# Kernel tuning notes

Hardware: AMD Instinct MI355X
Metric: run time of the kernel (lower is better)

The kernel has to match this reference:

```python
import jax, jax.numpy as jnp
import numpy as np

B, H, S, DK, DV = 2, 8, 2048, 64, 64


def _alibi_bias(num_heads, q_len, k_len, dtype=jnp.float32):
    # standard ALiBi slopes: 2^(-8h/H) for h = 1..H
    slopes = 2.0 ** (-8.0 * jnp.arange(1, num_heads + 1, dtype=dtype) / num_heads)
    # relative distance bias: -(i - j), zero on/above diagonal matters only pre-mask
    dist = jnp.arange(k_len, dtype=dtype)[None, :] - jnp.arange(q_len, dtype=dtype)[:, None]
    return (slopes[:, None, None] * dist[None, :, :])[None]  # (1, H, S, S)


def setup_inputs() -> dict:
    key = jax.random.key(0)
    kq, kk, kv = jax.random.split(key, 3)
    query = jax.random.normal(kq, (B, H, S, DK), dtype=jnp.float32)
    key_t = jax.random.normal(kk, (B, H, S, DK), dtype=jnp.float32)
    value = jax.random.normal(kv, (B, H, S, DV), dtype=jnp.float32)
    # causal mask: positions with 1 are masked (j > i)
    mask = jnp.triu(jnp.ones((S, S), dtype=jnp.int32), k=1)[None, None]  # (1,1,S,S)
    alibi_bias = _alibi_bias(H, S, S)  # (1,H,S,S)
    return {"query": query, "key": key_t, "value": value, "mask": mask, "alibi_bias": alibi_bias}


def reference(query, key, value, mask, alibi_bias):
    d_k = query.shape[-1]
    scale = 1.0 / jnp.sqrt(jnp.asarray(d_k, dtype=jnp.float32))
    # scores: (B, H, S, S)
    scores = jnp.einsum("bhqd,bhkd->bhqk", query, key) * scale
    scores = scores + alibi_bias
    scores = jnp.where(mask == 1, -jnp.inf, scores)
    attention_weights = jax.nn.softmax(scores, axis=-1)
    output = jnp.einsum("bhqk,bhkd->bhqd", attention_weights, value)
    return output, attention_weights
```

## Files before the change

### kernel.cpp

```cpp
#include <hip/hip_runtime.h>
#include <math.h>

#define BB 2
#define HH 8
#define SS 2048
#define DD 64
#define NBH (BB*HH)

typedef float f32x4 __attribute__((ext_vector_type(4)));
typedef short bf16x8 __attribute__((ext_vector_type(8)));
typedef short bf16x4 __attribute__((ext_vector_type(4)));

static __device__ __forceinline__ short f2bf(float x) {
    unsigned u = __float_as_uint(x);
    u = (u + 0x7fffu + ((u >> 16) & 1u)) >> 16;
    return (short)u;
}

__global__ __launch_bounds__(256) void prep_qk(const float* __restrict__ Q,
                                               const float* __restrict__ K,
                                               short* __restrict__ Qb,
                                               short* __restrict__ Kb)
{
    const int n4 = NBH * SS * DD / 4;
    for (int idx = blockIdx.x * 256 + threadIdx.x; idx < n4; idx += gridDim.x * 256) {
        float4 q = ((const float4*)Q)[idx];
        float4 k = ((const float4*)K)[idx];
        bf16x4 qo, ko;
        qo[0] = f2bf(0.125f * q.x); qo[1] = f2bf(0.125f * q.y);
        qo[2] = f2bf(0.125f * q.z); qo[3] = f2bf(0.125f * q.w);
        ko[0] = f2bf(k.x); ko[1] = f2bf(k.y); ko[2] = f2bf(k.z); ko[3] = f2bf(k.w);
        ((bf16x4*)Qb)[idx] = qo;
        ((bf16x4*)Kb)[idx] = ko;
    }
}

__global__ __launch_bounds__(256) void prep_vt(const float* __restrict__ V,
                                               short* __restrict__ Vt)
{
    __shared__ short t[64][72];
    const int jt = blockIdx.x, bh = blockIdx.y;
    const int tid = threadIdx.x;
    const int r  = tid >> 2;
    const int c4 = (tid & 3) * 16;
    const float* vb = V + ((size_t)bh * SS + (size_t)jt * 64) * DD;
    #pragma unroll
    for (int cc = 0; cc < 4; ++cc) {
        float4 v = *(const float4*)(vb + r * DD + c4 + cc * 4);
        t[c4 + cc*4 + 0][r] = f2bf(v.x);
        t[c4 + cc*4 + 1][r] = f2bf(v.y);
        t[c4 + cc*4 + 2][r] = f2bf(v.z);
        t[c4 + cc*4 + 3][r] = f2bf(v.w);
    }
    __syncthreads();
    short* ob = Vt + ((size_t)bh * DD + r) * SS + (size_t)jt * 64 + c4;
    *(bf16x8*)ob       = *(bf16x8*)&t[r][c4];
    *(bf16x8*)(ob + 8) = *(bf16x8*)&t[r][c4 + 8];
}

__global__ __launch_bounds__(512, 4) void attn_main(
    const short* __restrict__ Qb, const short* __restrict__ Kb,
    const short* __restrict__ Vt,
    float* __restrict__ out, float* __restrict__ wts)
{
    const int flat = blockIdx.x;
    const int wg   = (flat & 7) * 128 + (flat >> 3);
    const int bh   = wg >> 6;
    const int t_   = wg & 63;
    const int qt   = (t_ < 32) ? t_ : 95 - t_;
    const int q0   = qt * 32;
    const int h    = bh & 7;

    const int tid  = threadIdx.x;
    const int wv   = tid >> 6;
    const int lane = tid & 63;
    const int g    = lane >> 4;
    const int c16  = lane & 15;

    __shared__ float smo[8][16][65];
    __shared__ float lred[8][2][16];

    const short* Qp = Qb + ((size_t)bh * SS + q0) * DD;
    const short* Kp = Kb + (size_t)bh * SS * DD;
    const short* Vp = Vt + (size_t)bh * DD * SS;
    float* wbase = wts + ((size_t)bh * SS + q0) * (size_t)SS;
    float* obase = out + ((size_t)bh * SS + q0) * DD;

    const float slope  = exp2f(-(float)(h + 1));
    const int   nsteps = qt + 1;
    const int   cover  = q0 + 32;

    {
        const int n4 = (SS - cover) >> 2;
        const f32x4 z = {0.f, 0.f, 0.f, 0.f};
        for (int r = 0; r < 32; ++r) {
            float* wr = wbase + (size_t)r * SS + cover;
            for (int c = tid; c < n4; c += 512) ((f32x4*)wr)[c] = z;
        }
    }

    bf16x8 qf[2][2];
    #pragma unroll
    for (int qh = 0; qh < 2; ++qh)
        #pragma unroll
        for (int c = 0; c < 2; ++c)
            qf[qh][c] = *(const bf16x8*)(Qp + (size_t)(qh*16 + c16) * DD + c*32 + g*8);

    int kk8[8]; float offc[8];
    #pragma unroll
    for (int t = 0; t < 2; ++t)
        #pragma unroll
        for (int r = 0; r < 4; ++r) {
            kk8[t*4+r]  = 16*t + 4*g + r;
            offc[t*4+r] = slope * (float)(16*t + 4*g + r);
        }

    float l[2] = {0.f, 0.f};
    for (int s = wv; s < nsteps; s += 8) {
        const int j0 = s * 32;
        bf16x8 kf[2][2];
        #pragma unroll
        for (int t = 0; t < 2; ++t)
            #pragma unroll
            for (int c = 0; c < 2; ++c)
                kf[t][c] = *(const bf16x8*)(Kp + (size_t)(j0 + 16*t + c16) * DD + c*32 + g*8);

        f32x4 acc[2][2];
        #pragma unroll
        for (int qh = 0; qh < 2; ++qh)
            #pragma unroll
            for (int t = 0; t < 2; ++t)
                acc[qh][t] = (f32x4){0.f, 0.f, 0.f, 0.f};
        #pragma unroll
        for (int qh = 0; qh < 2; ++qh)
            #pragma unroll
            for (int t = 0; t < 2; ++t)
                #pragma unroll
                for (int c = 0; c < 2; ++c)
                    acc[qh][t] = __builtin_amdgcn_mfma_f32_16x16x32_bf16(kf[t][c], qf[qh][c], acc[qh][t], 0, 0, 0);

        const bool diag = (s == qt);
        #pragma unroll
        for (int qh = 0; qh < 2; ++qh) {
            const int   irow = q0 + qh*16 + c16;
            const float sb   = slope * (float)(j0 - irow);
            const int   lim  = irow - j0;
            float ls = 0.f;
            #pragma unroll
            for (int u = 0; u < 8; ++u) {
                float e = __expf(acc[qh][u>>2][u&3] + sb + offc[u]);
                if (diag) e = (kk8[u] <= lim) ? e : 0.f;
                ls += e;
            }
            l[qh] += ls;
        }
    }
    #pragma unroll
    for (int qh = 0; qh < 2; ++qh) {
        l[qh] += __shfl_xor(l[qh], 16, 64);
        l[qh] += __shfl_xor(l[qh], 32, 64);
    }

    if (lane < 16) {
        #pragma unroll
        for (int qh = 0; qh < 2; ++qh) lred[wv][qh][lane] = l[qh];
    }
    __syncthreads();
    float invl[2];
    #pragma unroll
    for (int qh = 0; qh < 2; ++qh) {
        float lf = 0.f;
        #pragma unroll
        for (int w2 = 0; w2 < 8; ++w2) lf += lred[w2][qh][c16];
        invl[qh] = 1.f / lf;
    }

    f32x4 oacc[2][4];
    #pragma unroll
    for (int qh = 0; qh < 2; ++qh)
        #pragma unroll
        for (int d0 = 0; d0 < 4; ++d0) oacc[qh][d0] = (f32x4){0.f, 0.f, 0.f, 0.f};

    for (int s = wv; s < nsteps; s += 8) {
        const int j0 = s * 32;
        bf16x8 kf[2][2];
        #pragma unroll
        for (int t = 0; t < 2; ++t)
            #pragma unroll
            for (int c = 0; c < 2; ++c)
                kf[t][c] = *(const bf16x8*)(Kp + (size_t)(j0 + 16*t + c16) * DD + c*32 + g*8);

        f32x4 acc[2][2];
        #pragma unroll
        for (int qh = 0; qh < 2; ++qh)
            #pragma unroll
            for (int t = 0; t < 2; ++t)
                acc[qh][t] = (f32x4){0.f, 0.f, 0.f, 0.f};
        #pragma unroll
        for (int qh = 0; qh < 2; ++qh)
            #pragma unroll
            for (int t = 0; t < 2; ++t)
                #pragma unroll
                for (int c = 0; c < 2; ++c)
                    acc[qh][t] = __builtin_amdgcn_mfma_f32_16x16x32_bf16(kf[t][c], qf[qh][c], acc[qh][t], 0, 0, 0);

        const bool diag = (s == qt);
        bf16x8 wf[2];
        #pragma unroll
        for (int qh = 0; qh < 2; ++qh) {
            const int   irow = q0 + qh*16 + c16;
            const float sb   = slope * (float)(j0 - irow);
            const int   lim  = irow - j0;
            float w8[8];
            #pragma unroll
            for (int u = 0; u < 8; ++u) {
                float e = __expf(acc[qh][u>>2][u&3] + sb + offc[u]);
                if (diag) e = (kk8[u] <= lim) ? e : 0.f;
                w8[u] = e * invl[qh];
            }
            float* wr0 = wbase + (size_t)(qh*16 + c16) * SS + j0 + 4*g;
            *(f32x4*)wr0        = (f32x4){w8[0], w8[1], w8[2], w8[3]};
            *(f32x4*)(wr0 + 16) = (f32x4){w8[4], w8[5], w8[6], w8[7]};
            #pragma unroll
            for (int u = 0; u < 8; ++u) wf[qh][u] = f2bf(w8[u]);
        }

        const short* vp = Vp + j0;
        #pragma unroll
        for (int d0 = 0; d0 < 4; ++d0) {
            const short* vr = vp + (size_t)(d0*16 + c16) * SS;
            bf16x4 a  = *(const bf16x4*)(vr + 4*g);
            bf16x4 b2 = *(const bf16x4*)(vr + 16 + 4*g);
            bf16x8 vf;
            vf[0]=a[0]; vf[1]=a[1]; vf[2]=a[2]; vf[3]=a[3];
            vf[4]=b2[0]; vf[5]=b2[1]; vf[6]=b2[2]; vf[7]=b2[3];
            #pragma unroll
            for (int qh = 0; qh < 2; ++qh)
                oacc[qh][d0] = __builtin_amdgcn_mfma_f32_16x16x32_bf16(vf, wf[qh], oacc[qh][d0], 0, 0, 0);
        }
    }

    __syncthreads();
    #pragma unroll
    for (int qh = 0; qh < 2; ++qh) {
        #pragma unroll
        for (int d0 = 0; d0 < 4; ++d0)
            *(f32x4*)&smo[wv][c16][d0*16 + 4*g] = oacc[qh][d0];
        __syncthreads();
        if (tid < 256) {
            int q = tid >> 4, dc = tid & 15;
            f32x4 r = {0.f, 0.f, 0.f, 0.f};
            #pragma unroll
            for (int w2 = 0; w2 < 8; ++w2) r += *(f32x4*)&smo[w2][q][dc * 4];
            *(f32x4*)(obase + (size_t)(qh*16 + q) * DD + dc * 4) = r;
        }
        __syncthreads();
    }
}

extern "C" void kernel_launch(void* const* d_in, const int* in_sizes, int n_in,
                              void* d_out, int out_size, void* d_ws, size_t ws_size,
                              hipStream_t stream) {
    const float* Q = (const float*)d_in[0];
    const float* K = (const float*)d_in[1];
    const float* V = (const float*)d_in[2];

    float* out = (float*)d_out;
    float* wts = out + (size_t)BB * HH * SS * DD;

    const size_t n = (size_t)NBH * SS * DD;
    short* Qb = (short*)d_ws;
    short* Kb = Qb + n;
    short* Vt = Kb + n;

    prep_qk<<<dim3(1024), dim3(256), 0, stream>>>(Q, K, Qb, Kb);
    prep_vt<<<dim3(SS / 64, NBH), dim3(256), 0, stream>>>(V, Vt);

    attn_main<<<dim3(1024), dim3(512), 0, stream>>>(Qb, Kb, Vt, out, wts);
}
```

Before: 120.7 us.

## Split query tiles into paired 16-row groups per workgroup

Each workgroup now processes two 16-row query groups (G and 127-G) sequentially instead of one 32-row tile, rebalancing causal work at finer granularity. Per-step computation handles a single 16-row Q fragment, reducing register pressure. In exchange, K and V fragments are reused across fewer rows, and the kernel adds an extra pass with its own synchronizations and partially masked diagonal blocks.

```diff
diff --git a/kernel.cpp b/kernel.cpp
--- a/kernel.cpp
+++ b/kernel.cpp
@@ -66,9 +66,7 @@
     const int flat = blockIdx.x;
     const int wg   = (flat & 7) * 128 + (flat >> 3);
     const int bh   = wg >> 6;
-    const int t_   = wg & 63;
-    const int qt   = (t_ < 32) ? t_ : 95 - t_;
-    const int q0   = qt * 32;
+    const int slot = wg & 63;
     const int h    = bh & 7;
 
     const int tid  = threadIdx.x;
@@ -78,33 +76,12 @@
     const int c16  = lane & 15;
 
     __shared__ float smo[8][16][65];
-    __shared__ float lred[8][2][16];
-
-    const short* Qp = Qb + ((size_t)bh * SS + q0) * DD;
+    __shared__ float lred[8][16];
+
     const short* Kp = Kb + (size_t)bh * SS * DD;
     const short* Vp = Vt + (size_t)bh * DD * SS;
-    float* wbase = wts + ((size_t)bh * SS + q0) * (size_t)SS;
-    float* obase = out + ((size_t)bh * SS + q0) * DD;
-
-    const float slope  = exp2f(-(float)(h + 1));
-    const int   nsteps = qt + 1;
-    const int   cover  = q0 + 32;
-
-    {
-        const int n4 = (SS - cover) >> 2;
-        const f32x4 z = {0.f, 0.f, 0.f, 0.f};
-        for (int r = 0; r < 32; ++r) {
-            float* wr = wbase + (size_t)r * SS + cover;
-            for (int c = tid; c < n4; c += 512) ((f32x4*)wr)[c] = z;
-        }
-    }
-
-    bf16x8 qf[2][2];
-    #pragma unroll
-    for (int qh = 0; qh < 2; ++qh)
-        #pragma unroll
-        for (int c = 0; c < 2; ++c)
-            qf[qh][c] = *(const bf16x8*)(Qp + (size_t)(qh*16 + c16) * DD + c*32 + g*8);
+
+    const float slope = exp2f(-(float)(h + 1));
 
     int kk8[8]; float offc[8];
     #pragma unroll
@@ -115,144 +92,137 @@
             offc[t*4+r] = slope * (float)(16*t + 4*g + r);
         }
 
-    float l[2] = {0.f, 0.f};
-    for (int s = wv; s < nsteps; s += 8) {
-        const int j0 = s * 32;
-        bf16x8 kf[2][2];
-        #pragma unroll
-        for (int t = 0; t < 2; ++t)
-            #pragma unroll
-            for (int c = 0; c < 2; ++c)
-                kf[t][c] = *(const bf16x8*)(Kp + (size_t)(j0 + 16*t + c16) * DD + c*32 + g*8);
-
-        f32x4 acc[2][2];
-        #pragma unroll
-        for (int qh = 0; qh < 2; ++qh)
-            #pragma unroll
-            for (int t = 0; t < 2; ++t)
-                acc[qh][t] = (f32x4){0.f, 0.f, 0.f, 0.f};
-        #pragma unroll
-        for (int qh = 0; qh < 2; ++qh)
-            #pragma unroll
-            for (int t = 0; t < 2; ++t)
-                #pragma unroll
-                for (int c = 0; c < 2; ++c)
-                    acc[qh][t] = __builtin_amdgcn_mfma_f32_16x16x32_bf16(kf[t][c], qf[qh][c], acc[qh][t], 0, 0, 0);
-
-        const bool diag = (s == qt);
-        #pragma unroll
-        for (int qh = 0; qh < 2; ++qh) {
-            const int   irow = q0 + qh*16 + c16;
-            const float sb   = slope * (float)(j0 - irow);
-            const int   lim  = irow - j0;
+    #pragma unroll 1
+    for (int it = 0; it < 2; ++it) {
+        const int G      = (it == 0) ? slot : 127 - slot;
+        const int q0     = G * 16;
+        const int nsteps = (G >> 1) + 1;
+        const int cover  = nsteps * 32;
+        const int irow   = q0 + c16;
+
+        const short* Qp = Qb + ((size_t)bh * SS + q0) * DD;
+        float* wbase = wts + ((size_t)bh * SS + q0) * (size_t)SS;
+        float* obase = out + ((size_t)bh * SS + q0) * DD;
+
+        {
+            const int n4 = (SS - cover) >> 2;
+            const f32x4 z = {0.f, 0.f, 0.f, 0.f};
+            for (int r = 0; r < 16; ++r) {
+                float* wr = wbase + (size_t)r * SS + cover;
+                for (int c = tid; c < n4; c += 512) ((f32x4*)wr)[c] = z;
+            }
+        }
+
+        bf16x8 qf[2];
+        #pragma unroll
+        for (int c = 0; c < 2; ++c)
+            qf[c] = *(const bf16x8*)(Qp + (size_t)c16 * DD + c*32 + g*8);
+
+        float l = 0.f;
+        for (int s = wv; s < nsteps; s += 8) {
+            const int j0 = s * 32;
+            bf16x8 kf[2][2];
+            #pragma unroll
+            for (int t = 0; t < 2; ++t)
+                #pragma unroll
+                for (int c = 0; c < 2; ++c)
+                    kf[t][c] = *(const bf16x8*)(Kp + (size_t)(j0 + 16*t + c16) * DD + c*32 + g*8);
+
+            f32x4 acc[2];
+            acc[0] = (f32x4){0.f,0.f,0.f,0.f};
+            acc[1] = (f32x4){0.f,0.f,0.f,0.f};
+            #pragma unroll
+            for (int t = 0; t < 2; ++t)
+                #pragma unroll
+                for (int c = 0; c < 2; ++c)
+                    acc[t] = __builtin_amdgcn_mfma_f32_16x16x32_bf16(kf[t][c], qf[c], acc[t], 0, 0, 0);
+
+            const bool diag = (s == nsteps - 1);
+            const float sb  = slope * (float)(j0 - irow);
+            const int   lim = irow - j0;
             float ls = 0.f;
             #pragma unroll
             for (int u = 0; u < 8; ++u) {
-                float e = __expf(acc[qh][u>>2][u&3] + sb + offc[u]);
+                float e = __expf(acc[u>>2][u&3] + sb + offc[u]);
                 if (diag) e = (kk8[u] <= lim) ? e : 0.f;
                 ls += e;
             }
-            l[qh] += ls;
-        }
-    }
-    #pragma unroll
-    for (int qh = 0; qh < 2; ++qh) {
-        l[qh] += __shfl_xor(l[qh], 16, 64);
-        l[qh] += __shfl_xor(l[qh], 32, 64);
-    }
-
-    if (lane < 16) {
-        #pragma unroll
-        for (int qh = 0; qh < 2; ++qh) lred[wv][qh][lane] = l[qh];
-    }
-    __syncthreads();
-    float invl[2];
-    #pragma unroll
-    for (int qh = 0; qh < 2; ++qh) {
+            l += ls;
+        }
+        l += __shfl_xor(l, 16, 64);
+        l += __shfl_xor(l, 32, 64);
+
+        if (lane < 16) lred[wv][lane] = l;
+        __syncthreads();
         float lf = 0.f;
         #pragma unroll
-        for (int w2 = 0; w2 < 8; ++w2) lf += lred[w2][qh][c16];
-        invl[qh] = 1.f / lf;
-    }
-
-    f32x4 oacc[2][4];
-    #pragma unroll
-    for (int qh = 0; qh < 2; ++qh)
-        #pragma unroll
-        for (int d0 = 0; d0 < 4; ++d0) oacc[qh][d0] = (f32x4){0.f, 0.f, 0.f, 0.f};
-
-    for (int s = wv; s < nsteps; s += 8) {
-        const int j0 = s * 32;
-        bf16x8 kf[2][2];
-        #pragma unroll
-        for (int t = 0; t < 2; ++t)
-            #pragma unroll
-            for (int c = 0; c < 2; ++c)
-                kf[t][c] = *(const bf16x8*)(Kp + (size_t)(j0 + 16*t + c16) * DD + c*32 + g*8);
-
-        f32x4 acc[2][2];
-        #pragma unroll
-        for (int qh = 0; qh < 2; ++qh)
-            #pragma unroll
-            for (int t = 0; t < 2; ++t)
-                acc[qh][t] = (f32x4){0.f, 0.f, 0.f, 0.f};
-        #pragma unroll
-        for (int qh = 0; qh < 2; ++qh)
-            #pragma unroll
-            for (int t = 0; t < 2; ++t)
-                #pragma unroll
-                for (int c = 0; c < 2; ++c)
-                    acc[qh][t] = __builtin_amdgcn_mfma_f32_16x16x32_bf16(kf[t][c], qf[qh][c], acc[qh][t], 0, 0, 0);
-
-        const bool diag = (s == qt);
-        bf16x8 wf[2];
-        #pragma unroll
-        for (int qh = 0; qh < 2; ++qh) {
-            const int   irow = q0 + qh*16 + c16;
-            const float sb   = slope * (float)(j0 - irow);
-            const int   lim  = irow - j0;
+        for (int w2 = 0; w2 < 8; ++w2) lf += lred[w2][c16];
+        const float invl = 1.f / lf;
+
+        f32x4 oacc[4];
+        #pragma unroll
+        for (int d0 = 0; d0 < 4; ++d0) oacc[d0] = (f32x4){0.f,0.f,0.f,0.f};
+
+        for (int s = wv; s < nsteps; s += 8) {
+            const int j0 = s * 32;
+            bf16x8 kf[2][2];
+            #pragma unroll
+            for (int t = 0; t < 2; ++t)
+                #pragma unroll
+                for (int c = 0; c < 2; ++c)
+                    kf[t][c] = *(const bf16x8*)(Kp + (size_t)(j0 + 16*t + c16) * DD + c*32 + g*8);
+
+            f32x4 acc[2];
+            acc[0] = (f32x4){0.f,0.f,0.f,0.f};
+            acc[1] = (f32x4){0.f,0.f,0.f,0.f};
+            #pragma unroll
+            for (int t = 0; t < 2; ++t)
+                #pragma unroll
+                for (int c = 0; c < 2; ++c)
+                    acc[t] = __builtin_amdgcn_mfma_f32_16x16x32_bf16(kf[t][c], qf[c], acc[t], 0, 0, 0);
+
+            const bool diag = (s == nsteps - 1);
+            const float sb  = slope * (float)(j0 - irow);
+            const int   lim = irow - j0;
             float w8[8];
             #pragma unroll
             for (int u = 0; u < 8; ++u) {
-                float e = __expf(acc[qh][u>>2][u&3] + sb + offc[u]);
+                float e = __expf(acc[u>>2][u&3] + sb + offc[u]);
                 if (diag) e = (kk8[u] <= lim) ? e : 0.f;
-                w8[u] = e * invl[qh];
-            }
-            float* wr0 = wbase + (size_t)(qh*16 + c16) * SS + j0 + 4*g;
+                w8[u] = e * invl;
+            }
+            float* wr0 = wbase + (size_t)c16 * SS + j0 + 4*g;
             *(f32x4*)wr0        = (f32x4){w8[0], w8[1], w8[2], w8[3]};
             *(f32x4*)(wr0 + 16) = (f32x4){w8[4], w8[5], w8[6], w8[7]};
-            #pragma unroll
-            for (int u = 0; u < 8; ++u) wf[qh][u] = f2bf(w8[u]);
-        }
-
-        const short* vp = Vp + j0;
-        #pragma unroll
-        for (int d0 = 0; d0 < 4; ++d0) {
-            const short* vr = vp + (size_t)(d0*16 + c16) * SS;
-            bf16x4 a  = *(const bf16x4*)(vr + 4*g);
-            bf16x4 b2 = *(const bf16x4*)(vr + 16 + 4*g);
-            bf16x8 vf;
-            vf[0]=a[0]; vf[1]=a[1]; vf[2]=a[2]; vf[3]=a[3];
-            vf[4]=b2[0]; vf[5]=b2[1]; vf[6]=b2[2]; vf[7]=b2[3];
-            #pragma unroll
-            for (int qh = 0; qh < 2; ++qh)
-                oacc[qh][d0] = __builtin_amdgcn_mfma_f32_16x16x32_bf16(vf, wf[qh], oacc[qh][d0], 0, 0, 0);
-        }
-    }
-
-    __syncthreads();
-    #pragma unroll
-    for (int qh = 0; qh < 2; ++qh) {
+
+            bf16x8 wf;
+            #pragma unroll
+            for (int u = 0; u < 8; ++u) wf[u] = f2bf(w8[u]);
+
+            const short* vp = Vp + j0;
+            #pragma unroll
+            for (int d0 = 0; d0 < 4; ++d0) {
+                const short* vr = vp + (size_t)(d0*16 + c16) * SS;
+                bf16x4 a  = *(const bf16x4*)(vr + 4*g);
+                bf16x4 b2 = *(const bf16x4*)(vr + 16 + 4*g);
+                bf16x8 vf;
+                vf[0]=a[0]; vf[1]=a[1]; vf[2]=a[2]; vf[3]=a[3];
+                vf[4]=b2[0]; vf[5]=b2[1]; vf[6]=b2[2]; vf[7]=b2[3];
+                oacc[d0] = __builtin_amdgcn_mfma_f32_16x16x32_bf16(vf, wf, oacc[d0], 0, 0, 0);
+            }
+        }
+
+        __syncthreads();
         #pragma unroll
         for (int d0 = 0; d0 < 4; ++d0)
-            *(f32x4*)&smo[wv][c16][d0*16 + 4*g] = oacc[qh][d0];
+            *(f32x4*)&smo[wv][c16][d0*16 + 4*g] = oacc[d0];
         __syncthreads();
         if (tid < 256) {
             int q = tid >> 4, dc = tid & 15;
             f32x4 r = {0.f, 0.f, 0.f, 0.f};
             #pragma unroll
             for (int w2 = 0; w2 < 8; ++w2) r += *(f32x4*)&smo[w2][q][dc * 4];
-            *(f32x4*)(obase + (size_t)(qh*16 + q) * DD + dc * 4) = r;
+            *(f32x4*)(obase + (size_t)q * DD + dc * 4) = r;
         }
         __syncthreads();
     }
```

Result: slower. 155.1 us (+28.5%).
